# Optimization experiments

Measured on AMD Instinct MI355X. Metric: run time of the kernel, lower is better.

Reference implementation:

```python
import jax, jax.numpy as jnp
import numpy as np
from functools import partial

B, S, V, H, NH, NKV, M, L = 2, 2048, 51200, 1536, 24, 4, 8960, 8
DH = H // NH  # 64
EPS = 1e-6


def setup_inputs() -> dict:
    key = jax.random.key(0)
    ks = jax.random.split(key, 16)
    sc = 0.02
    w = lambda k, shape: jax.random.normal(k, shape, jnp.float32) * sc
    inp = {
        "input_ids": jax.random.randint(ks[0], (B, S), 0, V),
        "attention_mask": jnp.ones((B, S), jnp.float32),
        "embed": w(ks[1], (V, H)),
        "Wq": w(ks[2], (L, H, H)),          "bq": jnp.zeros((L, H), jnp.float32),
        "Wk": w(ks[3], (L, H, NKV * DH)),   "bk": jnp.zeros((L, NKV * DH), jnp.float32),
        "Wv": w(ks[4], (L, H, NKV * DH)),   "bv": jnp.zeros((L, NKV * DH), jnp.float32),
        "Wo": w(ks[5], (L, H, H)),
        "ln1": jnp.ones((L, H), jnp.float32),
        "ln2": jnp.ones((L, H), jnp.float32),
        "Wg": w(ks[6], (L, H, M)),
        "Wu": w(ks[7], (L, H, M)),
        "Wd": w(ks[8], (L, M, H)),
        "norm_w": jnp.ones((H,), jnp.float32),
        "W1": w(ks[9], (H, H)), "b1": jnp.zeros((H,), jnp.float32),
        "W2": w(ks[10], (H, 1)), "b2": jnp.zeros((1,), jnp.float32),
    }
    inv_freq = 1.0 / (10000.0 ** (jnp.arange(0, DH, 2, dtype=jnp.float32) / DH))
    freqs = jnp.outer(jnp.arange(S, dtype=jnp.float32), inv_freq)  # [S, DH/2]
    emb = jnp.concatenate([freqs, freqs], axis=-1)                 # [S, DH]
    inp["cos"] = jnp.cos(emb)
    inp["sin"] = jnp.sin(emb)
    return inp


def _rms(x, w):
    var = jnp.mean(x.astype(jnp.float32) ** 2, axis=-1, keepdims=True)
    return w * (x * jax.lax.rsqrt(var + EPS)).astype(x.dtype)


def _rotate_half(x):
    x1, x2 = jnp.split(x, 2, axis=-1)
    return jnp.concatenate([-x2, x1], axis=-1)


def _forward(input_ids, attention_mask, embed, Wq, bq, Wk, bk, Wv, bv, Wo,
             ln1, ln2, Wg, Wu, Wd, norm_w, W1, b1, W2, b2, cos, sin):
    scale = 1.0 / np.sqrt(DH)
    b, s = input_ids.shape
    c = cos[None, :s, None, :]  # [1,S,1,DH]
    sn = sin[None, :s, None, :]
    rope = lambda t: t * c + _rotate_half(t) * sn
    mask0 = attention_mask[:, None, None, :] == 0  # [B,1,1,S]

    def block(x, p):
        wq, bq_, wk, bk_, wv, bv_, wo, ln1w, ln2w, wg, wu, wd = p
        h = _rms(x, ln1w)
        q = (h @ wq + bq_).reshape(b, s, NH, DH)
        k = (h @ wk + bk_).reshape(b, s, NKV, DH)
        v = (h @ wv + bv_).reshape(b, s, NKV, DH)
        q, k = rope(q), rope(k)
        k = jnp.repeat(k, NH // NKV, axis=2)  # GQA expand to NH heads
        v = jnp.repeat(v, NH // NKV, axis=2)
        scores = jnp.einsum('bqhd,bkhd->bhqk', q, k) * scale
        scores = jnp.where(mask0, -1e10, scores)
        probs = jax.nn.softmax(scores, axis=-1)  # dropout: eval mode (identity)
        attn = jnp.einsum('bhqk,bkhd->bqhd', probs, v).reshape(b, s, H)
        x = x + attn @ wo
        h = _rms(x, ln2w)
        x = x + (jax.nn.sigmoid(h @ wg) * (h @ wu)) @ wd
        return x, None

    x = embed[input_ids]  # [B,S,H]
    x, _ = jax.lax.scan(block, x, (Wq, bq, Wk, bk, Wv, bv, Wo, ln1, ln2, Wg, Wu, Wd))
    x = _rms(x, norm_w)
    h = jax.nn.gelu(x @ W1 + b1, approximate=False)  # torch nn.GELU default = exact
    return h @ W2 + b2  # [B,S,1]


def reference(input_ids, attention_mask, embed, Wq, bq, Wk, bk, Wv, bv, Wo,
              ln1, ln2, Wg, Wu, Wd, norm_w, W1, b1, W2, b2, cos, sin):
    return _forward(input_ids, attention_mask, embed, Wq, bq, Wk, bk, Wv, bv, Wo,
                    ln1, ln2, Wg, Wu, Wd, norm_w, W1, b1, W2, b2, cos, sin)
```

## Files before the change

### kernel.cpp

```cpp
#include <hip/hip_runtime.h>

typedef float f32x4 __attribute__((ext_vector_type(4)));
typedef short s16x8 __attribute__((ext_vector_type(8)));
typedef unsigned short u16;
typedef unsigned short u16x4 __attribute__((ext_vector_type(4)));
typedef unsigned short u16x8 __attribute__((ext_vector_type(8)));

__device__ __forceinline__ float bf2f(u16 u){ union{unsigned int i; float f;} v; v.i=((unsigned int)u)<<16; return v.f; }
__device__ __forceinline__ u16 f2bf(float f){ union{float f; unsigned int i;} v; v.f=f; return (u16)((v.i + 0x7FFFu + ((v.i>>16)&1u))>>16); }

__device__ __forceinline__ void gld16(const void* gp, void* lp){
  __builtin_amdgcn_global_load_lds((__attribute__((address_space(1))) void*)(void*)gp,
                                   (__attribute__((address_space(3))) void*)lp, 16, 0, 0);
}

__global__ __launch_bounds__(256) void k_embed(const int* __restrict__ ids, const float* __restrict__ emb, float* __restrict__ x){
  int r = blockIdx.x;
  int id = ids[r];
  const f32x4* src = (const f32x4*)(emb + (size_t)id*1536);
  f32x4* dst = (f32x4*)(x + (size_t)r*1536);
  for (int i = threadIdx.x; i < 384; i += 256) dst[i] = src[i];
}

__global__ __launch_bounds__(256) void k_rms(const float* __restrict__ x, const float* __restrict__ w, u16* __restrict__ h){
  int r = blockIdx.x, tid = threadIdx.x;
  const f32x4* xr = (const f32x4*)(x + (size_t)r*1536);
  f32x4 v0 = xr[tid];
  float ss = v0.x*v0.x + v0.y*v0.y + v0.z*v0.z + v0.w*v0.w;
  f32x4 v1 = {0,0,0,0};
  if (tid < 128){ v1 = xr[256+tid]; ss += v1.x*v1.x + v1.y*v1.y + v1.z*v1.z + v1.w*v1.w; }
  #pragma unroll
  for (int off=32; off; off>>=1) ss += __shfl_xor(ss, off, 64);
  __shared__ float red[4];
  if ((tid&63)==0) red[tid>>6] = ss;
  __syncthreads();
  float tot = red[0]+red[1]+red[2]+red[3];
  float invr = rsqrtf(tot*(1.f/1536.f) + 1e-6f);
  const f32x4* w4 = (const f32x4*)w;
  u16x4* h4 = (u16x4*)(h + (size_t)r*1536);
  {
    f32x4 wv = w4[tid];
    u16x4 o; o.x=f2bf(v0.x*invr*wv.x); o.y=f2bf(v0.y*invr*wv.y); o.z=f2bf(v0.z*invr*wv.z); o.w=f2bf(v0.w*invr*wv.w);
    h4[tid] = o;
  }
  if (tid < 128){
    f32x4 wv = w4[256+tid];
    u16x4 o; o.x=f2bf(v1.x*invr*wv.x); o.y=f2bf(v1.y*invr*wv.y); o.z=f2bf(v1.z*invr*wv.z); o.w=f2bf(v1.w*invr*wv.w);
    h4[256+tid] = o;
  }
}

__global__ __launch_bounds__(256) void k_rms_add(float* __restrict__ x, const float* __restrict__ P, const float* __restrict__ w, u16* __restrict__ h){
  int r = blockIdx.x, tid = threadIdx.x;
  f32x4* xr = (f32x4*)(x + (size_t)r*1536);
  const f32x4* pr = (const f32x4*)(P + (size_t)r*1536);
  f32x4 v0 = xr[tid], p0 = pr[tid];
  v0.x+=p0.x; v0.y+=p0.y; v0.z+=p0.z; v0.w+=p0.w;
  xr[tid] = v0;
  float ss = v0.x*v0.x + v0.y*v0.y + v0.z*v0.z + v0.w*v0.w;
  f32x4 v1 = {0,0,0,0};
  if (tid < 128){
    v1 = xr[256+tid]; f32x4 p1 = pr[256+tid];
    v1.x+=p1.x; v1.y+=p1.y; v1.z+=p1.z; v1.w+=p1.w;
    xr[256+tid] = v1;
    ss += v1.x*v1.x + v1.y*v1.y + v1.z*v1.z + v1.w*v1.w;
  }
  #pragma unroll
  for (int off=32; off; off>>=1) ss += __shfl_xor(ss, off, 64);
  __shared__ float red[4];
  if ((tid&63)==0) red[tid>>6] = ss;
  __syncthreads();
  float tot = red[0]+red[1]+red[2]+red[3];
  float invr = rsqrtf(tot*(1.f/1536.f) + 1e-6f);
  const f32x4* w4 = (const f32x4*)w;
  u16x4* h4 = (u16x4*)(h + (size_t)r*1536);
  {
    f32x4 wv = w4[tid];
    u16x4 o; o.x=f2bf(v0.x*invr*wv.x); o.y=f2bf(v0.y*invr*wv.y); o.z=f2bf(v0.z*invr*wv.z); o.w=f2bf(v0.w*invr*wv.w);
    h4[tid] = o;
  }
  if (tid < 128){
    f32x4 wv = w4[256+tid];
    u16x4 o; o.x=f2bf(v1.x*invr*wv.x); o.y=f2bf(v1.y*invr*wv.y); o.z=f2bf(v1.z*invr*wv.z); o.w=f2bf(v1.w*invr*wv.w);
    h4[256+tid] = o;
  }
}

__device__ __forceinline__ void cvt_tile(const float* src, int K, int N, u16* dst, int k0, int n0, int roff, int mode){
  __shared__ float T[64*72];
  int tid = threadIdx.x;
  #pragma unroll
  for (int j=0;j<4;++j){
    int i = tid + j*256;
    int row = i>>4, nf = i&15;
    f32x4 vv = *(const f32x4*)(src + (size_t)(k0+row)*N + n0 + nf*4);
    *(f32x4*)&T[row*72 + nf*4] = vv;
  }
  __syncthreads();
  #pragma unroll
  for (int j=0;j<2;++j){
    int i = tid + j*256;
    int n = i>>3, kc = i&7;
    u16x8 o;
    #pragma unroll
    for (int m=0;m<8;++m) o[m] = f2bf(T[(kc*8+m)*72 + n]);
    int gn = n0 + n;
    int dr = (mode==0) ? (roff + gn) : (((gn>>4)<<5) + ((mode==2)?16:0) + (gn&15));
    *(u16x8*)(dst + (size_t)dr*K + k0 + kc*8) = o;
  }
}

__global__ __launch_bounds__(256) void k_cvt_layer(
  const float* __restrict__ Wq, const float* __restrict__ Wk, const float* __restrict__ Wv,
  const float* __restrict__ Wo, const float* __restrict__ Wg, const float* __restrict__ Wu,
  const float* __restrict__ Wd, u16* qkvt, u16* wot, u16* gut, u16* wdt)
{
  const float* src; int K, N; u16* dst; int roff=0, mode=0;
  switch (blockIdx.y){
    case 0: src=Wq; K=1536; N=1536; dst=qkvt; break;
    case 1: src=Wk; K=1536; N=256;  dst=qkvt; roff=1536; break;
    case 2: src=Wv; K=1536; N=256;  dst=qkvt; roff=1792; break;
    case 3: src=Wo; K=1536; N=1536; dst=wot;  break;
    case 4: src=Wg; K=1536; N=8960; dst=gut;  mode=1; break;
    case 5: src=Wu; K=1536; N=8960; dst=gut;  mode=2; break;
    default: src=Wd; K=8960; N=1536; dst=wdt; break;
  }
  int ntn = N>>6;
  int nt = (K>>6)*ntn;
  int t = blockIdx.x;
  if (t >= nt) return;
  cvt_tile(src, K, N, dst, (t/ntn)<<6, (t%ntn)<<6, roff, mode);
}

__global__ __launch_bounds__(256) void k_cvt_one(const float* __restrict__ src, u16* __restrict__ dst){
  int t = blockIdx.x;
  cvt_tile(src, 1536, 1536, dst, (t/24)<<6, (t%24)<<6, 0, 0);
}

#define MODE_QKV 0
#define MODE_WO 1
#define MODE_GATEUP 2
#define MODE_DOWN 3
#define MODE_W1 4

template<int MODE>
__global__ __launch_bounds__(256) void k_gemm(
  const u16* __restrict__ A, const u16* __restrict__ Bt, int K,
  int jobsPerXcd, int nc, int ksplit, int klen,
  const float* __restrict__ bq_, const float* __restrict__ bk_, const float* __restrict__ bv_,
  float* __restrict__ xio, float* __restrict__ Pf,
  const float* __restrict__ cosT, const float* __restrict__ sinT,
  u16* __restrict__ o0, u16* __restrict__ o1, u16* __restrict__ o2)
{
  int bid = blockIdx.x;
  int xcd = bid & 7, j = bid >> 3;
  int job = xcd*jobsPerXcd + (j >> 5);
  if (job >= nc*ksplit) return;
  int rowb = j & 31;
  int col = job / ksplit;
  int ks  = job - col*ksplit;
  int kbase = ks*klen;
  int nt = klen >> 5;

  __shared__ __align__(16) u16 As[4][4096], Bs[4][4096];
  int tid = threadIdx.x;
  int lane = tid & 63, w = tid >> 6;
  int wr = w >> 1, wc = w & 1;
  int row0 = rowb * 128, col0 = col * 128;
  int l15 = lane & 15, l4 = lane >> 4;
  f32x4 acc[4][4] = {};
  const u16* aBase = A + (size_t)row0*K;
  const u16* bBase = Bt + (size_t)col0*K;
  int rr0 = tid & 127, kb0 = tid >> 7;
  int kb1 = kb0 + 2;

  auto stage = [&](int bf, int kt){
    gld16(aBase + (size_t)rr0*K + kt + kb0*8, &As[bf][tid*8]);
    gld16(bBase + (size_t)rr0*K + kt + kb0*8, &Bs[bf][tid*8]);
    gld16(aBase + (size_t)rr0*K + kt + kb1*8, &As[bf][(256+tid)*8]);
    gld16(bBase + (size_t)rr0*K + kt + kb1*8, &Bs[bf][(256+tid)*8]);
  };
  stage(0, kbase); stage(1, kbase+32); stage(2, kbase+64);

  for (int t = 0; t < nt; ++t){
    if (t < nt-2)       asm volatile("s_waitcnt vmcnt(8)" ::: "memory");
    else if (t == nt-2) asm volatile("s_waitcnt vmcnt(4)" ::: "memory");
    else                asm volatile("s_waitcnt vmcnt(0)" ::: "memory");
    __builtin_amdgcn_s_barrier();
    __builtin_amdgcn_sched_barrier(0);
    if (t+3 < nt) stage((t+3)&3, kbase + (t+3)*32);
    const u16* Ab = As[t&3];
    const u16* Bb = Bs[t&3];
    s16x8 af[4], bf_[4];
    #pragma unroll
    for (int i=0;i<4;++i) af[i]  = *(const s16x8*)&Ab[((l4<<7) + wr*64 + i*16 + l15)*8];
    #pragma unroll
    for (int jj=0;jj<4;++jj) bf_[jj] = *(const s16x8*)&Bb[((l4<<7) + wc*64 + jj*16 + l15)*8];
    __builtin_amdgcn_s_setprio(1);
    #pragma unroll
    for (int i=0;i<4;++i)
      #pragma unroll
      for (int jj=0;jj<4;++jj)
        acc[i][jj] = __builtin_amdgcn_mfma_f32_16x16x32_bf16(af[i], bf_[jj], acc[i][jj], 0, 0, 0);
    __builtin_amdgcn_s_setprio(0);
  }

  #pragma unroll
  for (int i=0;i<4;++i)
    #pragma unroll
    for (int jj=0;jj<4;++jj)
      #pragma unroll
      for (int r=0;r<4;++r){
        int row = row0 + wr*64 + i*16 + l4*4 + r;
        int c   = col0 + wc*64 + jj*16 + l15;
        float v = acc[i][jj][r];
        if constexpr (MODE == MODE_QKV){
          int b = row >> 11, s = row & 2047;
          if (c < 1536){
            int d = c & 63, hd = c >> 6;
            float vv = v + bq_[c];
            float pv = acc[i][jj^2][r] + bq_[c^32];
            float cv = cosT[s*64+d], sv = sinT[s*64+d];
            float sgn = (d<32) ? -1.f : 1.f;
            float o = (vv*cv + sgn*pv*sv)*0.125f;
            o0[(size_t)(b*24+hd)*131072 + (size_t)(s>>6)*4096
               + (s&63)*64 + (((d>>3)^(s&7))<<3) + (d&7)] = f2bf(o);
          } else if (c < 1792){
            int c2 = c - 1536, d = c2 & 63, kv = c2 >> 6;
            float vv = v + bk_[c2];
            float pv = acc[i][jj^2][r] + bk_[c2^32];
            float cv = cosT[s*64+d], sv = sinT[s*64+d];
            float sgn = (d<32) ? -1.f : 1.f;
            float o = vv*cv + sgn*pv*sv;
            o1[(size_t)(b*4+kv)*131072 + (size_t)(s>>6)*4096
               + (s&63)*64 + (((d>>3)^(s&7))<<3) + (d&7)] = f2bf(o);
          } else {
            int c2 = c - 1792, d = c2 & 63, kv = c2 >> 6;
            float vv = v + bv_[c2];
            o2[(size_t)(b*4+kv)*131072 + (size_t)(s>>6)*4096
               + d*64 + ((((s>>3)&7)^(d&7))<<3) + (s&7)] = f2bf(vv);
          }
        } else if constexpr (MODE == MODE_WO){
          xio[(size_t)row*1536 + c] += v;
        } else if constexpr (MODE == MODE_W1){
          v += bq_[c];
          float ge = 0.5f * v * (1.f + erff(v * 0.70710678118f));
          o0[(size_t)row*1536 + c] = f2bf(ge);
        }
      }
}

template<int MODE>
__global__ __launch_bounds__(512,2) void k_gemm256(
  const u16* __restrict__ A, const u16* __restrict__ Bt, int K,
  int nrt, int ksplit, int klen,
  float* __restrict__ xio, float* __restrict__ Pf, u16* __restrict__ o0)
{
  int bid = blockIdx.x;
  int wgid = (bid & 7)*(gridDim.x >> 3) + (bid >> 3);
  int nj = nrt*ksplit;
  int ct = wgid / nj; int r2 = wgid - ct*nj;
  int rt = r2 / ksplit; int ks = r2 - rt*ksplit;

  __shared__ __align__(16) u16 lds[2][2][16384];
  int tid = threadIdx.x;
  int lane = tid & 63, wid = tid >> 6;
  int wm = wid >> 2, wn = wid & 3;
  int l15 = lane & 15, l4 = lane >> 4;
  int row0 = rt*256, col0 = ct*256;
  int kbase = ks*klen*64;

  const u16* aB = A  + (size_t)row0*K + kbase;
  const u16* bB = Bt + (size_t)col0*K + kbase;
  int rsub = tid >> 3;
  int gsw  = (lane & 7) ^ ((lane >> 3) & 7);

  f32x4 acc[8][4] = {};

  auto stage = [&](int bf, int ktElem){
    #pragma unroll
    for (int a_=0; a_<4; ++a_){
      gld16(aB + (size_t)(a_*64 + rsub)*K + ktElem + gsw*8, &lds[bf][0][(a_*512+tid)*8]);
      gld16(bB + (size_t)(a_*64 + rsub)*K + ktElem + gsw*8, &lds[bf][1][(a_*512+tid)*8]);
    }
  };

  stage(0, 0);
  for (int t = 0; t < klen; ++t){
    asm volatile("s_waitcnt vmcnt(0)" ::: "memory");
    __builtin_amdgcn_s_barrier();
    __builtin_amdgcn_sched_barrier(0);
    if (t+1 < klen) stage((t+1)&1, (t+1)*64);
    const u16* Ab = lds[t&1][0];
    const u16* Bb = lds[t&1][1];
    #pragma unroll
    for (int ksu=0; ksu<2; ++ksu){
      s16x8 af[8], bf_[4];
      #pragma unroll
      for (int i=0;i<8;++i){
        int r = wm*128 + i*16 + l15;
        af[i] = *(const s16x8*)&Ab[r*64 + (((ksu*4 + l4) ^ (l15&7))*8)];
      }
      #pragma unroll
      for (int j=0;j<4;++j){
        int c = wn*64 + j*16 + l15;
        bf_[j] = *(const s16x8*)&Bb[c*64 + (((ksu*4 + l4) ^ (l15&7))*8)];
      }
      __builtin_amdgcn_s_setprio(1);
      #pragma unroll
      for (int i=0;i<8;++i)
        #pragma unroll
        for (int j=0;j<4;++j)
          acc[i][j] = __builtin_amdgcn_mfma_f32_16x16x32_bf16(af[i], bf_[j], acc[i][j], 0, 0, 0);
      __builtin_amdgcn_s_setprio(0);
    }
  }

  if constexpr (MODE == MODE_GATEUP){
    #pragma unroll
    for (int i=0;i<8;++i)
      #pragma unroll
      for (int j2=0;j2<4;j2+=2)
        #pragma unroll
        for (int r=0;r<4;++r){
          int row = row0 + wm*128 + i*16 + l4*4 + r;
          int cp  = col0 + wn*64 + j2*16 + l15;
          float gv = acc[i][j2][r], uv = acc[i][j2+1][r];
          float sg = 1.f/(1.f + __expf(-gv));
          int n = ((cp>>5)<<4) + (cp&15);
          o0[(size_t)row*8960 + n] = f2bf(sg*uv);
        }
  } else {
    #pragma unroll
    for (int i=0;i<8;++i)
      #pragma unroll
      for (int j=0;j<4;++j)
        #pragma unroll
        for (int r=0;r<4;++r){
          int row = row0 + wm*128 + i*16 + l4*4 + r;
          int c   = col0 + wn*64 + j*16 + l15;
          float v = acc[i][j][r];
          if (ks == 0) Pf[(size_t)row*1536 + c] = v;
          else         xio[(size_t)row*1536 + c] += v;
        }
  }
}

#define MFIX 4.0f
__global__ __launch_bounds__(256) void k_attn(
  const u16* __restrict__ q, const u16* __restrict__ k, const u16* __restrict__ v,
  const float* __restrict__ mask, u16* __restrict__ attn)
{
  __shared__ __align__(16) u16 Qs[4096];
  __shared__ __align__(16) u16 Kd[3][4096];
  __shared__ __align__(16) u16 Vd[3][4096];
  __shared__ __align__(16) u16 Ps[4][1024];
  __shared__ u16 Msh[2048];
  int tid = threadIdx.x;
  int lane = tid & 63, w = tid >> 6;
  int qb = blockIdx.x;
  int bh = blockIdx.y;
  int b = bh / 24, hh = bh % 24, kv = hh / 6;
  int l15 = lane & 15, l4 = lane >> 4;
  int sw = l15 & 7;

  const u16* qhead = q + ((size_t)(b*24 + hh))*131072 + qb*4096;
  const u16* khead = k + ((size_t)(b*4  + kv))*131072;
  const u16* vhead = v + ((size_t)(b*4  + kv))*131072;

  {
    const f32x4* m4 = (const f32x4*)(mask + b*2048);
    for (int i = tid; i < 512; i += 256){
      f32x4 mv = m4[i];
      u16x4 o;
      o.x = f2bf(mv.x==0.f ? -1e9f : 0.f);
      o.y = f2bf(mv.y==0.f ? -1e9f : 0.f);
      o.z = f2bf(mv.z==0.f ? -1e9f : 0.f);
      o.w = f2bf(mv.w==0.f ? -1e9f : 0.f);
      *(u16x4*)&Msh[i*4] = o;
    }
  }
  gld16(qhead + tid*8,       &Qs[tid*8]);
  gld16(qhead + (256+tid)*8, &Qs[(256+tid)*8]);

  auto stage = [&](int bf, int kt){
    gld16(khead + kt*4096 + tid*8,       &Kd[bf][tid*8]);
    gld16(khead + kt*4096 + (256+tid)*8, &Kd[bf][(256+tid)*8]);
    gld16(vhead + kt*4096 + tid*8,       &Vd[bf][tid*8]);
    gld16(vhead + kt*4096 + (256+tid)*8, &Vd[bf][(256+tid)*8]);
  };
  stage(0, 0);
  stage(1, 1);

  s16x8 aq0, aq1;
  f32x4 oacc[4] = {};
  float lsum = 0.f;
  u16* Pw = Ps[w];

  for (int t = 0; t < 32; ++t){
    if (t < 31) asm volatile("s_waitcnt vmcnt(4)" ::: "memory");
    else        asm volatile("s_waitcnt vmcnt(0)" ::: "memory");
    __builtin_amdgcn_s_barrier();
    __builtin_amdgcn_sched_barrier(0);
    if (t == 0){
      int qrow = w*16 + l15;
      aq0 = *(const s16x8*)&Qs[qrow*64 + (( l4    ^ sw)<<3)];
      aq1 = *(const s16x8*)&Qs[qrow*64 + (((4+l4) ^ sw)<<3)];
    }
    if (t+2 < 32) stage((t+2)%3, t+2);
    const u16* Kb = Kd[t%3];
    const u16* Vb = Vd[t%3];
    f32x4 sk[4] = {};
    __builtin_amdgcn_s_setprio(1);
    #pragma unroll
    for (int kn=0; kn<4; ++kn){
      int krow = kn*16 + l15;
      s16x8 a0 = *(const s16x8*)&Kb[krow*64 + (( l4    ^ sw)<<3)];
      s16x8 a1 = *(const s16x8*)&Kb[krow*64 + (((4+l4) ^ sw)<<3)];
      sk[kn] = __builtin_amdgcn_mfma_f32_16x16x32_bf16(a0, aq0, sk[kn], 0,0,0);
      sk[kn] = __builtin_amdgcn_mfma_f32_16x16x32_bf16(a1, aq1, sk[kn], 0,0,0);
    }
    __builtin_amdgcn_s_setprio(0);
    #pragma unroll
    for (int kn=0; kn<4; ++kn){
      u16x4 mv = *(const u16x4*)&Msh[t*64 + kn*16 + l4*4];
      u16x4 pk;
      #pragma unroll
      for (int r=0;r<4;++r){
        float p = __expf(sk[kn][r] + bf2f(mv[r]) - MFIX);
        lsum += p;
        pk[r] = f2bf(p);
      }
      int g = kn*2 + (l4>>1);
      *(u16x4*)&Pw[l15*64 + ((g ^ sw)<<3) + (l4&1)*4] = pk;
    }
    __builtin_amdgcn_s_setprio(1);
    #pragma unroll
    for (int ksu=0; ksu<2; ++ksu){
      s16x8 ap = *(const s16x8*)&Pw[l15*64 + (((ksu*4+l4) ^ sw)<<3)];
      #pragma unroll
      for (int dg=0; dg<4; ++dg){
        s16x8 bv = *(const s16x8*)&Vb[(dg*16+l15)*64 + (((ksu*4+l4) ^ sw)<<3)];
        oacc[dg] = __builtin_amdgcn_mfma_f32_16x16x32_bf16(ap, bv, oacc[dg], 0,0,0);
      }
    }
    __builtin_amdgcn_s_setprio(0);
  }
  lsum += __shfl_xor(lsum, 16, 64);
  lsum += __shfl_xor(lsum, 32, 64);
  float invq[4];
  #pragma unroll
  for (int r=0;r<4;++r) invq[r] = 1.f / __shfl(lsum, l4*4 + r, 64);
  #pragma unroll
  for (int dg=0;dg<4;++dg)
    #pragma unroll
    for (int r=0;r<4;++r){
      int token = b*2048 + qb*64 + w*16 + l4*4 + r;
      int col = hh*64 + dg*16 + l15;
      attn[(size_t)token*1536 + col] = f2bf(oacc[dg][r] * invq[r]);
    }
}

__global__ __launch_bounds__(256) void k_gemv(const u16* __restrict__ h2, const float* __restrict__ W2, const float* __restrict__ b2, float* __restrict__ out){
  int tid = threadIdx.x, lane = tid & 63, w = tid >> 6;
  int r = blockIdx.x*4 + w;
  const u16* hr = h2 + (size_t)r*1536;
  float s = 0.f;
  #pragma unroll
  for (int i=0;i<24;++i){ int c = lane + i*64; s += bf2f(hr[c]) * W2[c]; }
  #pragma unroll
  for (int off=32; off; off>>=1) s += __shfl_xor(s, off, 64);
  if (lane == 0) out[r] = s + b2[0];
}

extern "C" void kernel_launch(void* const* d_in, const int* in_sizes, int n_in,
                              void* d_out, int out_size, void* d_ws, size_t ws_size,
                              hipStream_t stream)
{
  const int*   ids   = (const int*)d_in[0];
  const float* mask  = (const float*)d_in[1];
  const float* embed = (const float*)d_in[2];
  const float* Wq    = (const float*)d_in[3];
  const float* bq    = (const float*)d_in[4];
  const float* Wk    = (const float*)d_in[5];
  const float* bk    = (const float*)d_in[6];
  const float* Wv    = (const float*)d_in[7];
  const float* bv    = (const float*)d_in[8];
  const float* Wo    = (const float*)d_in[9];
  const float* ln1   = (const float*)d_in[10];
  const float* ln2   = (const float*)d_in[11];
  const float* Wg    = (const float*)d_in[12];
  const float* Wu    = (const float*)d_in[13];
  const float* Wd    = (const float*)d_in[14];
  const float* nw    = (const float*)d_in[15];
  const float* W1    = (const float*)d_in[16];
  const float* b1    = (const float*)d_in[17];
  const float* W2    = (const float*)d_in[18];
  const float* b2    = (const float*)d_in[19];
  const float* cosT  = (const float*)d_in[20];
  const float* sinT  = (const float*)d_in[21];

  char* ws = (char*)d_ws;
  float* x   = (float*)(ws + 0);
  u16* h     = (u16*)(ws + 25165824);
  u16* qb_   = (u16*)(ws + 37748736);
  u16* kb_   = (u16*)(ws + 50331648);
  u16* vb_   = (u16*)(ws + 52428800);
  u16* attn  = (u16*)(ws + 54525952);
  u16* g     = (u16*)(ws + 67108864);
  u16* qkvt  = (u16*)(ws + 140509184);
  u16* wot   = (u16*)(ws + 146800640);
  u16* gut   = (u16*)(ws + 151519232);
  u16* wdt   = (u16*)(ws + 206569472);
  float* Pf  = (float*)(ws + 37748736);
  (void)in_sizes; (void)n_in; (void)out_size; (void)ws_size;

  k_embed<<<4096, 256, 0, stream>>>(ids, embed, x);
  for (int l = 0; l < 8; ++l){
    k_cvt_layer<<<dim3(3360,7), 256, 0, stream>>>(
      Wq + (size_t)l*1536*1536, Wk + (size_t)l*1536*256, Wv + (size_t)l*1536*256,
      Wo + (size_t)l*1536*1536, Wg + (size_t)l*1536*8960, Wu + (size_t)l*1536*8960,
      Wd + (size_t)l*8960*1536, qkvt, wot, gut, wdt);
    if (l == 0) k_rms<<<4096, 256, 0, stream>>>(x, ln1, h);
    else        k_rms_add<<<4096, 256, 0, stream>>>(x, Pf, ln1 + l*1536, h);
    k_gemm<MODE_QKV><<<512, 256, 0, stream>>>(h, qkvt, 1536, 2, 16, 1, 1536,
        bq + l*1536, bk + l*256, bv + l*256, nullptr, nullptr, cosT, sinT, qb_, kb_, vb_);
    k_attn<<<dim3(32,48), 256, 0, stream>>>(qb_, kb_, vb_, mask, attn);
    k_gemm<MODE_WO><<<512, 256, 0, stream>>>(attn, wot, 1536, 2, 12, 1, 1536,
        nullptr, nullptr, nullptr, x, nullptr, nullptr, nullptr, nullptr, nullptr, nullptr);
    k_rms<<<4096, 256, 0, stream>>>(x, ln2 + l*1536, h);
    k_gemm256<MODE_GATEUP><<<1120, 512, 0, stream>>>(h, gut, 1536, 16, 1, 24,
        nullptr, nullptr, g);
    k_gemm256<MODE_DOWN><<<192, 512, 0, stream>>>(g, wdt, 8960, 16, 2, 70,
        x, Pf, nullptr);
  }
  k_cvt_one<<<576, 256, 0, stream>>>(W1, wot);
  k_rms_add<<<4096, 256, 0, stream>>>(x, Pf, nw, h);
  k_gemm<MODE_W1><<<512, 256, 0, stream>>>(h, wot, 1536, 2, 12, 1, 1536,
      b1, nullptr, nullptr, nullptr, nullptr, nullptr, nullptr, attn, nullptr, nullptr);
  k_gemv<<<1024, 256, 0, stream>>>(attn, W2, b2, (float*)d_out);
}
```

Measured before the change: 5.675 ms.

## Fold log2e into Q scale, use raw exp2 and packed bf16 convert, shrink attention LDS

Q is pre-scaled by log2(e) in the QKV epilogue, and the fixed -4 offset is folded into the mask table. This lets the attention softmax use v_exp_f32 directly, with a hardware packed bf16 conversion instead of software rounding. The K/V ring buffer drops from triple to double buffering, and the P scratch reuses the Q shared buffer, cutting LDS use so more blocks can be resident. The cost is shallower prefetch, with a full vmcnt(0) wait every iteration.

```diff
diff --git a/kernel.cpp b/kernel.cpp
--- a/kernel.cpp
+++ b/kernel.cpp
@@ -5,9 +5,14 @@
 typedef unsigned short u16;
 typedef unsigned short u16x4 __attribute__((ext_vector_type(4)));
 typedef unsigned short u16x8 __attribute__((ext_vector_type(8)));
+typedef unsigned int u32x2 __attribute__((ext_vector_type(2)));
 
 __device__ __forceinline__ float bf2f(u16 u){ union{unsigned int i; float f;} v; v.i=((unsigned int)u)<<16; return v.f; }
 __device__ __forceinline__ u16 f2bf(float f){ union{float f; unsigned int i;} v; v.f=f; return (u16)((v.i + 0x7FFFu + ((v.i>>16)&1u))>>16); }
+__device__ __forceinline__ float aexp2(float x){ float r; asm("v_exp_f32 %0, %1" : "=v"(r) : "v"(x)); return r; }
+__device__ __forceinline__ unsigned int cvtpk(float lo, float hi){ unsigned int r; asm("v_cvt_pk_bf16_f32 %0, %1, %2" : "=v"(r) : "v"(lo), "v"(hi)); return r; }
+
+#define LOG2E 1.44269504089f
 
 __device__ __forceinline__ void gld16(const void* gp, void* lp){
   __builtin_amdgcn_global_load_lds((__attribute__((address_space(1))) void*)(void*)gp,
@@ -222,7 +227,7 @@
             float pv = acc[i][jj^2][r] + bq_[c^32];
             float cv = cosT[s*64+d], sv = sinT[s*64+d];
             float sgn = (d<32) ? -1.f : 1.f;
-            float o = (vv*cv + sgn*pv*sv)*0.125f;
+            float o = (vv*cv + sgn*pv*sv)*(0.125f*LOG2E);
             o0[(size_t)(b*24+hd)*131072 + (size_t)(s>>6)*4096
                + (s&63)*64 + (((d>>3)^(s&7))<<3) + (d&7)] = f2bf(o);
           } else if (c < 1792){
@@ -346,15 +351,13 @@
   }
 }
 
-#define MFIX 4.0f
 __global__ __launch_bounds__(256) void k_attn(
   const u16* __restrict__ q, const u16* __restrict__ k, const u16* __restrict__ v,
   const float* __restrict__ mask, u16* __restrict__ attn)
 {
   __shared__ __align__(16) u16 Qs[4096];
-  __shared__ __align__(16) u16 Kd[3][4096];
-  __shared__ __align__(16) u16 Vd[3][4096];
-  __shared__ __align__(16) u16 Ps[4][1024];
+  __shared__ __align__(16) u16 Kd[2][4096];
+  __shared__ __align__(16) u16 Vd[2][4096];
   __shared__ u16 Msh[2048];
   int tid = threadIdx.x;
   int lane = tid & 63, w = tid >> 6;
@@ -370,13 +373,15 @@
 
   {
     const f32x4* m4 = (const f32x4*)(mask + b*2048);
+    const u16 mvis = f2bf(-4.f*LOG2E);
+    const u16 mmask = f2bf(-1.4e9f);
     for (int i = tid; i < 512; i += 256){
       f32x4 mv = m4[i];
       u16x4 o;
-      o.x = f2bf(mv.x==0.f ? -1e9f : 0.f);
-      o.y = f2bf(mv.y==0.f ? -1e9f : 0.f);
-      o.z = f2bf(mv.z==0.f ? -1e9f : 0.f);
-      o.w = f2bf(mv.w==0.f ? -1e9f : 0.f);
+      o.x = (mv.x==0.f) ? mmask : mvis;
+      o.y = (mv.y==0.f) ? mmask : mvis;
+      o.z = (mv.z==0.f) ? mmask : mvis;
+      o.w = (mv.w==0.f) ? mmask : mvis;
       *(u16x4*)&Msh[i*4] = o;
     }
   }
@@ -390,16 +395,14 @@
     gld16(vhead + kt*4096 + (256+tid)*8, &Vd[bf][(256+tid)*8]);
   };
   stage(0, 0);
-  stage(1, 1);
 
   s16x8 aq0, aq1;
   f32x4 oacc[4] = {};
   float lsum = 0.f;
-  u16* Pw = Ps[w];
+  u16* Pw = &Qs[w*1024];
 
   for (int t = 0; t < 32; ++t){
-    if (t < 31) asm volatile("s_waitcnt vmcnt(4)" ::: "memory");
-    else        asm volatile("s_waitcnt vmcnt(0)" ::: "memory");
+    asm volatile("s_waitcnt vmcnt(0)" ::: "memory");
     __builtin_amdgcn_s_barrier();
     __builtin_amdgcn_sched_barrier(0);
     if (t == 0){
@@ -407,9 +410,9 @@
       aq0 = *(const s16x8*)&Qs[qrow*64 + (( l4    ^ sw)<<3)];
       aq1 = *(const s16x8*)&Qs[qrow*64 + (((4+l4) ^ sw)<<3)];
     }
-    if (t+2 < 32) stage((t+2)%3, t+2);
-    const u16* Kb = Kd[t%3];
-    const u16* Vb = Vd[t%3];
+    if (t+1 < 32) stage((t+1)&1, t+1);
+    const u16* Kb = Kd[t&1];
+    const u16* Vb = Vd[t&1];
     f32x4 sk[4] = {};
     __builtin_amdgcn_s_setprio(1);
     #pragma unroll
@@ -424,15 +427,14 @@
     #pragma unroll
     for (int kn=0; kn<4; ++kn){
       u16x4 mv = *(const u16x4*)&Msh[t*64 + kn*16 + l4*4];
-      u16x4 pk;
-      #pragma unroll
-      for (int r=0;r<4;++r){
-        float p = __expf(sk[kn][r] + bf2f(mv[r]) - MFIX);
-        lsum += p;
-        pk[r] = f2bf(p);
-      }
+      float p0 = aexp2(sk[kn][0] + bf2f(mv.x));
+      float p1 = aexp2(sk[kn][1] + bf2f(mv.y));
+      float p2 = aexp2(sk[kn][2] + bf2f(mv.z));
+      float p3 = aexp2(sk[kn][3] + bf2f(mv.w));
+      lsum += (p0 + p1) + (p2 + p3);
+      u32x2 pk; pk.x = cvtpk(p0, p1); pk.y = cvtpk(p2, p3);
       int g = kn*2 + (l4>>1);
-      *(u16x4*)&Pw[l15*64 + ((g ^ sw)<<3) + (l4&1)*4] = pk;
+      *(u32x2*)&Pw[l15*64 + ((g ^ sw)<<3) + (l4&1)*4] = pk;
     }
     __builtin_amdgcn_s_setprio(1);
     #pragma unroll
```

Measured after the change: 5.425 ms. -4.4%, faster.
